# Optimization experiments

Hardware: AMD Instinct MI355X
Metric: run time of the kernel (lower is better)

The kernel has to match this reference:

```python
import jax, jax.numpy as jnp
import numpy as np


def setup_inputs() -> dict:
    key = jax.random.key(0)
    ks = jax.random.split(key, 7)
    B, S, D, F, E = 4, 2048, 1024, 4096, 8
    scale = 0.02
    return {
        "x": jax.random.normal(ks[0], (B, S, D), dtype=jnp.float32),
        "gate_w": jax.random.normal(ks[1], (D, E), dtype=jnp.float32) * scale,
        "gate_b": jnp.zeros((E,), dtype=jnp.float32),
        "w1": jax.random.normal(ks[2], (E, D, F), dtype=jnp.float32) * scale,
        "b1": jnp.zeros((E, F), dtype=jnp.float32),
        "w2": jax.random.normal(ks[3], (E, F, D), dtype=jnp.float32) * scale,
        "b2": jnp.zeros((E, D), dtype=jnp.float32),
        "top_k": 2,
    }


def reference(x, gate_w, gate_b, w1, b1, w2, b2, top_k):
    B, S, D = x.shape
    E = w1.shape[0]
    xf = x.reshape(-1, D)                      # [T, D], T = B*S
    T = xf.shape[0]

    # Router: top-k logits, softmax over the selected k (as in torch code)
    logits = xf @ gate_w + gate_b              # [T, E]
    rw, sel = jax.lax.top_k(logits, top_k)     # [T, k], [T, k]
    w = jax.nn.softmax(rw, axis=-1)            # [T, k]

    # Dense combine weights: combine[t, e] = sum_k w[t,k] * (sel[t,k]==e)
    combine = jnp.zeros((T, E), dtype=xf.dtype)
    combine = combine.at[jnp.arange(T)[:, None], sel].add(w)

    # Loop over small fixed expert count; each expert FFN on all tokens,
    # weighted by combine (zero for unrouted tokens). Dropout p honored as 0 (eval).
    out = jnp.zeros_like(xf)
    for e in range(E):
        h = jax.nn.gelu(xf @ w1[e] + b1[e], approximate=False)  # torch F.gelu = exact
        out = out + combine[:, e:e + 1] * (h @ w2[e] + b2[e])
    return out.reshape(B, S, D)
```

## Files before the change

### kernel.cpp

```cpp
#include <hip/hip_runtime.h>
#include <math.h>

#define T_TOK 8192
#define DDIM  1024
#define FDIM  4096
#define NEXP  8
#define MT256 72
#define NSLOT (2 * T_TOK)
#define NG1   (16 * MT256)
#define NG2   (8 * MT256)

typedef __attribute__((ext_vector_type(8))) short short8;
typedef __attribute__((ext_vector_type(4))) float f32x4;
typedef __attribute__((ext_vector_type(4))) unsigned int u32x4;
typedef unsigned short u16;
typedef unsigned int   u32;

typedef const __attribute__((address_space(1))) u32* gp_t;
typedef       __attribute__((address_space(3))) u32* lp_t;

__device__ __forceinline__ void gload16(const void* g, void* l) {
  __builtin_amdgcn_global_load_lds((gp_t)g, (lp_t)l, 16, 0, 0);
}

#define VM2 asm volatile("s_waitcnt vmcnt(2)" ::: "memory")
#define VM0 asm volatile("s_waitcnt vmcnt(0)" ::: "memory")
#define SBAR __builtin_amdgcn_s_barrier()
#define SCHED0 __builtin_amdgcn_sched_barrier(0)

__device__ __forceinline__ u16 f2bf(float f) {
  u32 u = __float_as_uint(f);
  u = u + 0x7FFFu + ((u >> 16) & 1u);
  return (u16)(u >> 16);
}

__device__ __forceinline__ int imin(int a, int b) { return a < b ? a : b; }

__device__ __forceinline__ float gelu_fast(float v) {
  float u = 0.7978845608f * (v + 0.044715f * v * v * v);
  float t2 = __expf(2.f * u);
  float th = 1.f - 2.f / (t2 + 1.f);
  return 0.5f * v * (1.f + th);
}

__device__ __forceinline__ int xcd_swz(int orig, int nwg) {
  int xcd = orig & 7;
  int q = nwg >> 3, r = nwg & 7;
  int base = (xcd < r) ? xcd * (q + 1) : r * (q + 1) + (xcd - r) * q;
  return base + (orig >> 3);
}

__device__ void wtrans128(char* __restrict__ ldsb,
                          const float* __restrict__ in, u16* __restrict__ out,
                          int M, int N, int r0, int c0)
{
  const int tid = threadIdx.x;
  #pragma unroll
  for (int p = 0; p < 16; p++) {
    int r  = p * 8 + (tid >> 5);
    int c4 = (tid & 31) * 4;
    float4 v = *(const float4*)(in + (size_t)(r0 + r) * N + (c0 + c4));
    ushort4 o;
    o.x = f2bf(v.x); o.y = f2bf(v.y); o.z = f2bf(v.z); o.w = f2bf(v.w);
    *(ushort4*)(ldsb + r * 272 + (r >> 3) * 16 + c4 * 2) = o;
  }
  __syncthreads();
  #pragma unroll
  for (int p = 0; p < 8; p++) {
    int idx = p * 256 + tid;
    int c   = idx >> 4;
    int rg  = idx & 15;
    short8 o;
    #pragma unroll
    for (int j = 0; j < 8; j++) {
      int r = rg * 8 + j;
      o[j] = *(const short*)(ldsb + r * 272 + rg * 16 + c * 2);
    }
    __builtin_nontemporal_store(*(u32x4*)&o,
        (u32x4*)(out + (size_t)(c0 + c) * M + (r0 + rg * 8)));
  }
}

__global__ __launch_bounds__(256) void prep_kernel(
    const float* __restrict__ x, const float* __restrict__ gw,
    const float* __restrict__ gb, u16* __restrict__ xb,
    int* __restrict__ counts, int* __restrict__ sel, float* __restrict__ wts,
    const float* __restrict__ w1, u16* __restrict__ w1t,
    const float* __restrict__ w2, u16* __restrict__ w2t)
{
  __shared__ __align__(16) char ldsb[35072];
  const int b = blockIdx.x;
  if (b < 2048) {
    int e = b >> 8, rem = b & 255;
    int tm = rem >> 3, tn = rem & 7;
    wtrans128(ldsb, w2 + (size_t)e * FDIM * DDIM,
              w2t + (size_t)e * FDIM * DDIM, FDIM, DDIM, tm * 128, tn * 128);
    return;
  }
  if (b < 4096) {
    int tt = b - 2048;
    int e = tt >> 8, rem = tt & 255;
    int tm = rem & 7, tn = rem >> 3;
    wtrans128(ldsb, w1 + (size_t)e * DDIM * FDIM,
              w1t + (size_t)e * DDIM * FDIM, DDIM, FDIM, tm * 128, tn * 128);
    return;
  }
  float* gwT = (float*)ldsb;
  {
    const int tid = threadIdx.x;
    #pragma unroll
    for (int q = 0; q < 4; q++) {
      int d = q * 256 + tid;
      float4 a = *(const float4*)(gw + (size_t)d * NEXP);
      float4 c = *(const float4*)(gw + (size_t)d * NEXP + 4);
      gwT[0 * 1028 + d] = a.x; gwT[1 * 1028 + d] = a.y;
      gwT[2 * 1028 + d] = a.z; gwT[3 * 1028 + d] = a.w;
      gwT[4 * 1028 + d] = c.x; gwT[5 * 1028 + d] = c.y;
      gwT[6 * 1028 + d] = c.z; gwT[7 * 1028 + d] = c.w;
    }
  }
  __syncthreads();
  const int t    = (b - 4096) * 4 + (threadIdx.x >> 6);
  const int lane = threadIdx.x & 63;
  const float* xr = x + (size_t)t * DDIM;
  u16* xbr = xb + (size_t)t * DDIM;
  float lg[NEXP];
  #pragma unroll
  for (int e = 0; e < NEXP; e++) lg[e] = 0.f;
  #pragma unroll
  for (int i = 0; i < 4; i++) {
    int d0 = i * 256 + lane * 4;
    float4 v = *(const float4*)(xr + d0);
    ushort4 o;
    o.x = f2bf(v.x); o.y = f2bf(v.y); o.z = f2bf(v.z); o.w = f2bf(v.w);
    *(ushort4*)(xbr + d0) = o;
    #pragma unroll
    for (int e = 0; e < NEXP; e++) {
      float4 g4 = *(const float4*)&gwT[e * 1028 + d0];
      lg[e] += v.x * g4.x + v.y * g4.y + v.z * g4.z + v.w * g4.w;
    }
  }
  #pragma unroll
  for (int off = 32; off > 0; off >>= 1) {
    #pragma unroll
    for (int e = 0; e < NEXP; e++) lg[e] += __shfl_down(lg[e], off);
  }
  if (lane == 0) {
    float v0 = -1e30f, v1 = -1e30f; int s0 = 0, s1 = 0;
    #pragma unroll
    for (int e = 0; e < NEXP; e++) {
      float v = lg[e] + gb[e];
      if (v > v0) { v1 = v0; s1 = s0; v0 = v; s0 = e; }
      else if (v > v1) { v1 = v; s1 = e; }
    }
    float a  = expf(v1 - v0);
    float w0 = 1.f / (1.f + a);
    sel[t * 2] = s0; sel[t * 2 + 1] = s1;
    wts[t * 2] = w0; wts[t * 2 + 1] = 1.f - w0;
    atomicAdd(&counts[s0], 1); atomicAdd(&counts[s1], 1);
  }
}

__global__ __launch_bounds__(1024) void scan_assign_kernel(
    const int* __restrict__ counts, const int* __restrict__ sel,
    const float* __restrict__ wts,
    int* __restrict__ offsets, int* __restrict__ map_e, int* __restrict__ map_r,
    int* __restrict__ nT, int* __restrict__ stok, float* __restrict__ swgt)
{
  __shared__ int spos[NEXP];
  if (threadIdx.x == 0) {
    int run = 0, nt = 0;
    for (int e = 0; e < NEXP; e++) {
      offsets[e] = run; spos[e] = run;
      int c = counts[e];
      int ntile = (c + 255) >> 8;
      for (int i = 0; i < ntile; i++) { map_e[nt] = e; map_r[nt] = i * 256; nt++; }
      run += c;
    }
    nT[0] = nt;
  }
  __syncthreads();
  for (int t = threadIdx.x; t < T_TOK; t += 1024) {
    #pragma unroll
    for (int k = 0; k < 2; k++) {
      int e = sel[t * 2 + k];
      int p = atomicAdd(&spos[e], 1);
      stok[p] = t; swgt[p] = wts[t * 2 + k];
    }
  }
}

__global__ __launch_bounds__(1024, 4) void gemm1_kernel(
    const u16* __restrict__ xb, const int* __restrict__ slot_token,
    const u16* __restrict__ W1T, const float* __restrict__ B1,
    const int* __restrict__ counts, const int* __restrict__ offsets,
    const int* __restrict__ map_e, const int* __restrict__ map_r,
    const int* __restrict__ nT, u16* __restrict__ H)
{
  __shared__ __align__(16) char lds[3 * 32768];
  const int L     = xcd_swz(blockIdx.x, NG1);
  const int xg    = L / 144;
  const int local = L - xg * 144;
  const int tl    = local >> 4;
  const int n_idx = local & 15;
  const int t_idx = xg * 9 + tl;
  if (t_idx >= nT[0]) return;
  const int e    = map_e[t_idx];
  const int row0 = map_r[t_idx];
  const int cnt  = counts[e];
  const int off  = offsets[e];
  const int n0   = n_idx * 256;

  const int tid = threadIdx.x, wave = tid >> 6, lane = tid & 63;
  const int lr = lane & 15, lq = lane >> 4;
  const int wr = wave >> 2, wc = wave & 3;
  const int l2 = lane >> 2, lb = (lane & 3) * 16;

  const int R = wave * 16 + l2;
  int tok = slot_token[imin(off + row0 + R, NSLOT - 1)];
  if ((u32)tok >= T_TOK) tok = 0;
  const char* gA = (const char*)xb + (size_t)tok * 2048 + lb;
  const char* gB = (const char*)W1T + (size_t)(e * FDIM + n0 + R) * 2048 + lb;

  auto stage = [&](int slot, int k0) {
    char* base = lds + slot * 32768;
    gload16(gA + k0, base + wave * 1024 + lane * 16);
    gload16(gB + k0, base + 16384 + wave * 1024 + lane * 16);
  };

  f32x4 acc[4][4] = {};
  auto compute = [&](int slot) {
    const u16* As = (const u16*)(lds + slot * 32768);
    const u16* Bs = (const u16*)(lds + slot * 32768 + 16384);
    short8 a[4], bf[4];
    #pragma unroll
    for (int m = 0; m < 4; m++)
      a[m] = *(const short8*)&As[(wr * 64 + m * 16 + lr) * 32 + lq * 8];
    #pragma unroll
    for (int n = 0; n < 4; n++)
      bf[n] = *(const short8*)&Bs[(wc * 64 + n * 16 + lr) * 32 + lq * 8];
    #pragma unroll
    for (int m = 0; m < 4; m++)
      #pragma unroll
      for (int n = 0; n < 4; n++)
        acc[m][n] = __builtin_amdgcn_mfma_f32_16x16x32_bf16(a[m], bf[n], acc[m][n], 0, 0, 0);
  };

  stage(0, 0); stage(1, 64);
  VM2; SCHED0; SBAR; SCHED0;
  #pragma unroll 1
  for (int t = 0; t < 32; t++) {
    if (t + 2 < 32) stage((t + 2) % 3, (t + 2) * 64);
    compute(t % 3);
    SCHED0;
    if (t + 2 < 32)       { VM2; }
    else if (t + 2 == 32) { VM0; }
    SCHED0; SBAR; SCHED0;
  }

  #pragma unroll
  for (int nn = 0; nn < 4; nn++) {
    int col = n0 + wc * 64 + nn * 16 + lr;
    float b1v = B1[e * FDIM + col];
    #pragma unroll
    for (int m = 0; m < 4; m++) {
      int rbase = wr * 64 + m * 16 + lq * 4;
      #pragma unroll
      for (int j = 0; j < 4; j++) {
        int r = rbase + j;
        if (row0 + r < cnt) {
          float v = acc[m][nn][j] + b1v;
          H[(size_t)(off + row0 + r) * FDIM + col] = f2bf(gelu_fast(v));
        }
      }
    }
  }
}

__global__ __launch_bounds__(1024, 4) void gemm2_kernel(
    const u16* __restrict__ H, const u16* __restrict__ W2T,
    const float* __restrict__ B2,
    const int* __restrict__ counts, const int* __restrict__ offsets,
    const int* __restrict__ slot_token, const float* __restrict__ slot_weight,
    const int* __restrict__ map_e, const int* __restrict__ map_r,
    const int* __restrict__ nT, float* __restrict__ out)
{
  __shared__ __align__(16) char lds[3 * 32768];
  const int L     = xcd_swz(blockIdx.x, NG2);
  const int xg    = L / 72;
  const int local = L - xg * 72;
  const int tl    = local >> 3;
  const int combo = local & 7;
  const int sp    = combo >> 2;
  const int n_idx = combo & 3;
  const int t_idx = xg * 9 + tl;
  if (t_idx >= nT[0]) return;
  const int e    = map_e[t_idx];
  const int row0 = map_r[t_idx];
  const int cnt  = counts[e];
  const int off  = offsets[e];
  const int n0   = n_idx * 256;
  const int kbase = sp * 4096;

  const int tid = threadIdx.x, wave = tid >> 6, lane = tid & 63;
  const int lr = lane & 15, lq = lane >> 4;
  const int wr = wave >> 2, wc = wave & 3;
  const int l2 = lane >> 2, lb = (lane & 3) * 16;

  const int R = wave * 16 + l2;
  int aidx = imin(off + row0 + R, NSLOT - 1);
  const char* gA = (const char*)H + (size_t)aidx * 8192 + kbase + lb;
  const char* gB = (const char*)W2T + (size_t)(e * DDIM + n0 + R) * 8192 + kbase + lb;

  auto stage = [&](int slot, int k0) {
    char* base = lds + slot * 32768;
    gload16(gA + k0, base + wave * 1024 + lane * 16);
    gload16(gB + k0, base + 16384 + wave * 1024 + lane * 16);
  };

  f32x4 acc[4][4] = {};
  auto compute = [&](int slot) {
    const u16* As = (const u16*)(lds + slot * 32768);
    const u16* Bs = (const u16*)(lds + slot * 32768 + 16384);
    short8 a[4], bf[4];
    #pragma unroll
    for (int m = 0; m < 4; m++)
      a[m] = *(const short8*)&As[(wr * 64 + m * 16 + lr) * 32 + lq * 8];
    #pragma unroll
    for (int n = 0; n < 4; n++)
      bf[n] = *(const short8*)&Bs[(wc * 64 + n * 16 + lr) * 32 + lq * 8];
    #pragma unroll
    for (int m = 0; m < 4; m++)
      #pragma unroll
      for (int n = 0; n < 4; n++)
        acc[m][n] = __builtin_amdgcn_mfma_f32_16x16x32_bf16(a[m], bf[n], acc[m][n], 0, 0, 0);
  };

  stage(0, 0); stage(1, 64);
  VM2; SCHED0; SBAR; SCHED0;
  #pragma unroll 1
  for (int t = 0; t < 64; t++) {
    if (t + 2 < 64) stage((t + 2) % 3, (t + 2) * 64);
    compute(t % 3);
    SCHED0;
    if (t + 2 < 64)       { VM2; }
    else if (t + 2 == 64) { VM0; }
    SCHED0; SBAR; SCHED0;
  }

  #pragma unroll
  for (int m = 0; m < 4; m++) {
    int rbase = wr * 64 + m * 16 + lq * 4;
    #pragma unroll
    for (int j = 0; j < 4; j++) {
      int r = rbase + j;
      if (row0 + r >= cnt) continue;
      int s = off + row0 + r;
      int tok = slot_token[s];
      float wgt = slot_weight[s];
      #pragma unroll
      for (int n = 0; n < 4; n++) {
        int col = n0 + wc * 64 + n * 16 + lr;
        float v = acc[m][n][j];
        if (sp == 0) v += B2[e * DDIM + col];
        atomicAdd(&out[(size_t)tok * DDIM + col], wgt * v);
      }
    }
  }
}

extern "C" void kernel_launch(void* const* d_in, const int* in_sizes, int n_in,
                              void* d_out, int out_size, void* d_ws, size_t ws_size,
                              hipStream_t stream)
{
  (void)in_sizes; (void)n_in; (void)ws_size;
  const float* x  = (const float*)d_in[0];
  const float* gw = (const float*)d_in[1];
  const float* gb = (const float*)d_in[2];
  const float* w1 = (const float*)d_in[3];
  const float* b1 = (const float*)d_in[4];
  const float* w2 = (const float*)d_in[5];
  const float* b2 = (const float*)d_in[6];

  char* ws = (char*)d_ws;
  int*   counts = (int*)(ws + 0);
  int*   offp   = (int*)(ws + 64);
  int*   nT     = (int*)(ws + 128);
  int*   map_e  = (int*)(ws + 256);
  int*   map_r  = (int*)(ws + 1024);

  size_t p = 2048;
  int*   sel   = (int*)(ws + p);   p += (size_t)T_TOK * 2 * 4;
  float* wts   = (float*)(ws + p); p += (size_t)T_TOK * 2 * 4;
  int*   stok  = (int*)(ws + p);   p += (size_t)NSLOT * 4;
  float* swgt  = (float*)(ws + p); p += (size_t)NSLOT * 4;
  p = (p + 1048575) & ~(size_t)1048575;
  u16*   xb    = (u16*)(ws + p);   p += (size_t)T_TOK * DDIM * 2;
  u16*   w1t   = (u16*)(ws + p);   p += (size_t)NEXP * DDIM * FDIM * 2;
  u16*   w2t   = (u16*)(ws + p);   p += (size_t)NEXP * DDIM * FDIM * 2;
  u16*   Hbuf  = (u16*)(ws + p);

  hipMemsetAsync(ws, 0, 256, stream);
  hipMemsetAsync(d_out, 0, (size_t)out_size * sizeof(float), stream);
  prep_kernel<<<4096 + T_TOK / 4, 256, 0, stream>>>(
      x, gw, gb, xb, counts, sel, wts, w1, w1t, w2, w2t);
  scan_assign_kernel<<<1, 1024, 0, stream>>>(counts, sel, wts, offp, map_e, map_r, nT, stok, swgt);
  gemm1_kernel<<<NG1, 1024, 0, stream>>>(
      xb, stok, w1t, b1, counts, offp, map_e, map_r, nT, Hbuf);
  gemm2_kernel<<<NG2, 1024, 0, stream>>>(
      Hbuf, w2t, b2, counts, offp, stok, swgt, map_e, map_r, nT, (float*)d_out);
}
```

Before: 790.8 us.

## Move w2 transpose-convert from prep kernel into extra gemm1 blocks

The fp32-to-bf16 transpose of w2 now runs in 2048 extra 1024-thread blocks appended to the gemm1 grid instead of in the prep kernel, using a new transpose variant sized for 1024 threads. The goal is to hide this memory-bound conversion behind gemm1's compute-bound work and shorten the serial prep stage. In exchange, the transpose blocks compete with gemm1 for CUs and bandwidth, and with gemm1's large shared-memory footprint they may occupy slots badly or finish late, extending gemm1's tail.

```diff
diff --git a/kernel.cpp b/kernel.cpp
--- a/kernel.cpp
+++ b/kernel.cpp
@@ -9,6 +9,7 @@
 #define NSLOT (2 * T_TOK)
 #define NG1   (16 * MT256)
 #define NG2   (8 * MT256)
+#define NW2T  2048
 
 typedef __attribute__((ext_vector_type(8))) short short8;
 typedef __attribute__((ext_vector_type(4))) float f32x4;
@@ -81,25 +82,47 @@
   }
 }
 
+__device__ void wtrans128_w(char* __restrict__ ldsb,
+                            const float* __restrict__ in, u16* __restrict__ out,
+                            int M, int N, int r0, int c0)
+{
+  const int tid = threadIdx.x;
+  #pragma unroll
+  for (int p = 0; p < 4; p++) {
+    int r  = p * 32 + (tid >> 5);
+    int c4 = (tid & 31) * 4;
+    float4 v = *(const float4*)(in + (size_t)(r0 + r) * N + (c0 + c4));
+    ushort4 o;
+    o.x = f2bf(v.x); o.y = f2bf(v.y); o.z = f2bf(v.z); o.w = f2bf(v.w);
+    *(ushort4*)(ldsb + r * 272 + (r >> 3) * 16 + c4 * 2) = o;
+  }
+  __syncthreads();
+  #pragma unroll
+  for (int p = 0; p < 2; p++) {
+    int idx = p * 1024 + tid;
+    int c   = idx >> 4;
+    int rg  = idx & 15;
+    short8 o;
+    #pragma unroll
+    for (int j = 0; j < 8; j++) {
+      int r = rg * 8 + j;
+      o[j] = *(const short*)(ldsb + r * 272 + rg * 16 + c * 2);
+    }
+    __builtin_nontemporal_store(*(u32x4*)&o,
+        (u32x4*)(out + (size_t)(c0 + c) * M + (r0 + rg * 8)));
+  }
+}
+
 __global__ __launch_bounds__(256) void prep_kernel(
     const float* __restrict__ x, const float* __restrict__ gw,
     const float* __restrict__ gb, u16* __restrict__ xb,
     int* __restrict__ counts, int* __restrict__ sel, float* __restrict__ wts,
-    const float* __restrict__ w1, u16* __restrict__ w1t,
-    const float* __restrict__ w2, u16* __restrict__ w2t)
+    const float* __restrict__ w1, u16* __restrict__ w1t)
 {
   __shared__ __align__(16) char ldsb[35072];
   const int b = blockIdx.x;
   if (b < 2048) {
     int e = b >> 8, rem = b & 255;
-    int tm = rem >> 3, tn = rem & 7;
-    wtrans128(ldsb, w2 + (size_t)e * FDIM * DDIM,
-              w2t + (size_t)e * FDIM * DDIM, FDIM, DDIM, tm * 128, tn * 128);
-    return;
-  }
-  if (b < 4096) {
-    int tt = b - 2048;
-    int e = tt >> 8, rem = tt & 255;
     int tm = rem & 7, tn = rem >> 3;
     wtrans128(ldsb, w1 + (size_t)e * DDIM * FDIM,
               w1t + (size_t)e * DDIM * FDIM, DDIM, FDIM, tm * 128, tn * 128);
@@ -112,15 +135,15 @@
     for (int q = 0; q < 4; q++) {
       int d = q * 256 + tid;
       float4 a = *(const float4*)(gw + (size_t)d * NEXP);
-      float4 c = *(const float4*)(gw + (size_t)d * NEXP + 4);
+      float4 cc = *(const float4*)(gw + (size_t)d * NEXP + 4);
       gwT[0 * 1028 + d] = a.x; gwT[1 * 1028 + d] = a.y;
       gwT[2 * 1028 + d] = a.z; gwT[3 * 1028 + d] = a.w;
-      gwT[4 * 1028 + d] = c.x; gwT[5 * 1028 + d] = c.y;
-      gwT[6 * 1028 + d] = c.z; gwT[7 * 1028 + d] = c.w;
+      gwT[4 * 1028 + d] = cc.x; gwT[5 * 1028 + d] = cc.y;
+      gwT[6 * 1028 + d] = cc.z; gwT[7 * 1028 + d] = cc.w;
     }
   }
   __syncthreads();
-  const int t    = (b - 4096) * 4 + (threadIdx.x >> 6);
+  const int t    = (b - 2048) * 4 + (threadIdx.x >> 6);
   const int lane = threadIdx.x & 63;
   const float* xr = x + (size_t)t * DDIM;
   u16* xbr = xb + (size_t)t * DDIM;
@@ -195,9 +218,18 @@
     const u16* __restrict__ W1T, const float* __restrict__ B1,
     const int* __restrict__ counts, const int* __restrict__ offsets,
     const int* __restrict__ map_e, const int* __restrict__ map_r,
-    const int* __restrict__ nT, u16* __restrict__ H)
+    const int* __restrict__ nT, u16* __restrict__ H,
+    const float* __restrict__ w2, u16* __restrict__ w2t)
 {
   __shared__ __align__(16) char lds[3 * 32768];
+  if (blockIdx.x >= NG1) {
+    int b = blockIdx.x - NG1;
+    int e = b >> 8, rem = b & 255;
+    int tm = rem >> 3, tn = rem & 7;
+    wtrans128_w(lds, w2 + (size_t)e * FDIM * DDIM,
+                w2t + (size_t)e * FDIM * DDIM, FDIM, DDIM, tm * 128, tn * 128);
+    return;
+  }
   const int L     = xcd_swz(blockIdx.x, NG1);
   const int xg    = L / 144;
   const int local = L - xg * 144;
@@ -402,11 +434,11 @@
 
   hipMemsetAsync(ws, 0, 256, stream);
   hipMemsetAsync(d_out, 0, (size_t)out_size * sizeof(float), stream);
-  prep_kernel<<<4096 + T_TOK / 4, 256, 0, stream>>>(
-      x, gw, gb, xb, counts, sel, wts, w1, w1t, w2, w2t);
+  prep_kernel<<<2048 + T_TOK / 4, 256, 0, stream>>>(
+      x, gw, gb, xb, counts, sel, wts, w1, w1t);
   scan_assign_kernel<<<1, 1024, 0, stream>>>(counts, sel, wts, offp, map_e, map_r, nT, stok, swgt);
-  gemm1_kernel<<<NG1, 1024, 0, stream>>>(
-      xb, stok, w1t, b1, counts, offp, map_e, map_r, nT, Hbuf);
+  gemm1_kernel<<<NG1 + NW2T, 1024, 0, stream>>>(
+      xb, stok, w1t, b1, counts, offp, map_e, map_r, nT, Hbuf, w2, w2t);
   gemm2_kernel<<<NG2, 1024, 0, stream>>>(
       Hbuf, w2t, b2, counts, offp, stok, swgt, map_e, map_r, nT, (float*)d_out);
 }
```

Result: faster. 750.0 us (median of 2 runs) (-5.2%).
